# Kernel tuning notes

Measured on AMD Instinct MI355X. Metric: run time of the kernel, lower is better.

The kernel has to match this reference:

```python
import jax, jax.numpy as jnp
import numpy as np
import math

D_MODEL = 768
NHEAD = 12
NUM_LAYERS = 6
INPUT_DIM = 768
HEAD_DIM = D_MODEL // NHEAD
D_FF = 4 * D_MODEL
TOTAL_HEADS = NUM_LAYERS * NHEAD
B, N = 4, 512


def _ln(x, g, b, eps=1e-5):
    mu = jnp.mean(x, axis=-1, keepdims=True)
    var = jnp.mean((x - mu) ** 2, axis=-1, keepdims=True)
    return (x - mu) * jax.lax.rsqrt(var + eps) * g + b


def setup_inputs() -> dict:
    key = jax.random.key(0)
    ks = iter(jax.random.split(key, 32))
    s = 0.02  # init scale keeps sigmoid scores away from saturation
    d = {
        "sentence_embeddings": jax.random.normal(next(ks), (B, N, INPUT_DIM), jnp.float32),
        "Win": jax.random.normal(next(ks), (D_MODEL, INPUT_DIM), jnp.float32) * s,
        "b_in": jnp.zeros((D_MODEL,), jnp.float32),
        "Wq": jax.random.normal(next(ks), (NUM_LAYERS, D_MODEL, D_MODEL), jnp.float32) * s,
        "bq": jnp.zeros((NUM_LAYERS, D_MODEL), jnp.float32),
        "Wk": jax.random.normal(next(ks), (NUM_LAYERS, D_MODEL, D_MODEL), jnp.float32) * s,
        "bk": jnp.zeros((NUM_LAYERS, D_MODEL), jnp.float32),
        "Wv": jax.random.normal(next(ks), (NUM_LAYERS, D_MODEL, D_MODEL), jnp.float32) * s,
        "bv": jnp.zeros((NUM_LAYERS, D_MODEL), jnp.float32),
        "Wo": jax.random.normal(next(ks), (NUM_LAYERS, D_MODEL, D_MODEL), jnp.float32) * s,
        "bo": jnp.zeros((NUM_LAYERS, D_MODEL), jnp.float32),
        "g1": jnp.ones((NUM_LAYERS, D_MODEL), jnp.float32),
        "be1": jnp.zeros((NUM_LAYERS, D_MODEL), jnp.float32),
        "g2": jnp.ones((NUM_LAYERS, D_MODEL), jnp.float32),
        "be2": jnp.zeros((NUM_LAYERS, D_MODEL), jnp.float32),
        "W1": jax.random.normal(next(ks), (NUM_LAYERS, D_FF, D_MODEL), jnp.float32) * s,
        "bf1": jnp.zeros((NUM_LAYERS, D_FF), jnp.float32),
        "W2": jax.random.normal(next(ks), (NUM_LAYERS, D_MODEL, D_FF), jnp.float32) * s,
        "bf2": jnp.zeros((NUM_LAYERS, D_MODEL), jnp.float32),
        "Wr1": jax.random.normal(next(ks), (D_MODEL // 2, D_MODEL), jnp.float32) * s,
        "br1": jnp.zeros((D_MODEL // 2,), jnp.float32),
        "Wr2": jax.random.normal(next(ks), (TOTAL_HEADS, D_MODEL // 2), jnp.float32) * s,
        "br2": jnp.zeros((TOTAL_HEADS,), jnp.float32),
        "agg_bias": jnp.zeros((1,), jnp.float32),
    }
    return d


def _forward(sentence_embeddings, Win, b_in, Wq, bq, Wk, bk, Wv, bv, Wo, bo,
             g1, be1, g2, be2, W1, bf1, W2, bf2, Wr1, br1, Wr2, br2, agg_bias):
    b, n, _ = sentence_embeddings.shape
    x = sentence_embeddings @ Win.T + b_in  # [B,N,D]
    off_diag = (1.0 - jnp.eye(n, dtype=x.dtype))[None, None]  # [1,1,N,N]
    scale = 1.0 / math.sqrt(HEAD_DIM)
    all_scores = []
    for i in range(NUM_LAYERS):
        n1 = _ln(x, g1[i], be1[i])
        q = (n1 @ Wq[i].T + bq[i]).reshape(b, n, NHEAD, HEAD_DIM).transpose(0, 2, 1, 3)
        k = (n1 @ Wk[i].T + bk[i]).reshape(b, n, NHEAD, HEAD_DIM).transpose(0, 2, 1, 3)
        v = (n1 @ Wv[i].T + bv[i]).reshape(b, n, NHEAD, HEAD_DIM).transpose(0, 2, 1, 3)
        scores = jnp.einsum('bhnd,bhmd->bhnm', q, k) * scale
        probs = jax.nn.sigmoid(scores)  # [B,H,N,N]
        row_sums = probs.sum(axis=-1, keepdims=True) + 1e-6
        attn = jnp.einsum('bhnm,bhmd->bhnd', probs, v) / row_sums
        attn = attn.transpose(0, 2, 1, 3).reshape(b, n, D_MODEL)
        x = x + attn @ Wo[i].T + bo[i]
        n2 = _ln(x, g2[i], be2[i])
        ff = jax.nn.gelu(n2 @ W1[i].T + bf1[i], approximate=False) @ W2[i].T + bf2[i]
        x = x + ff
        all_scores.append(probs * off_diag)  # zero the diagonal
    raw_w = jax.nn.gelu(x @ Wr1.T + br1, approximate=False) @ Wr2.T + br2  # [B,N,LH]
    stacked = jnp.concatenate(all_scores, axis=1)  # [B, L*H, N, N]
    final = jnp.einsum('bnh,bhnm->bnm', raw_w, stacked)
    return final + agg_bias[0]


def reference(sentence_embeddings, Win, b_in, Wq, bq, Wk, bk, Wv, bv, Wo, bo,
              g1, be1, g2, be2, W1, bf1, W2, bf2, Wr1, br1, Wr2, br2, agg_bias):
    return _forward(sentence_embeddings, Win, b_in, Wq, bq, Wk, bk, Wv, bv, Wo, bo,
                    g1, be1, g2, be2, W1, bf1, W2, bf2, Wr1, br1, Wr2, br2, agg_bias)
```

## Files before the change

### kernel.cpp

```cpp
#include <hip/hip_runtime.h>
#include <stdint.h>

#define LAYERS 6
#define BB 4
#define NSEQ 512
#define DM 768
#define NH 12
#define HD 64
#define DFF 3072
#define MTOK 2048
#define QKVN 2304
#define DR1 384
#define TH 72

typedef __attribute__((ext_vector_type(8))) short bf16x8;
typedef __attribute__((ext_vector_type(4))) float f32x4;

__device__ __forceinline__ unsigned short f2bf(float f) {
  union { float f; uint32_t u; } v; v.f = f;
  return (unsigned short)((v.u + 0x7fffu + ((v.u >> 16) & 1u)) >> 16);
}
__device__ __forceinline__ float bf2f(unsigned short h) {
  union { uint32_t u; float f; } v; v.u = ((uint32_t)h) << 16;
  return v.f;
}
__device__ __forceinline__ void gload16(const void* g, void* l) {
  __builtin_amdgcn_global_load_lds((const __attribute__((address_space(1))) void*)g,
                                   (__attribute__((address_space(3))) void*)l, 16, 0, 0);
}
#define MFMA(a, b, c) __builtin_amdgcn_mfma_f32_16x16x32_bf16(a, b, c, 0, 0, 0)

__device__ __forceinline__ float sigmoid8(float s) {
  float e, r;
  float t = s * -0.18033688011112443f;
  asm("v_exp_f32 %0, %1" : "=v"(e) : "v"(t));
  float d = 1.0f + e;
  asm("v_rcp_f32 %0, %1" : "=v"(r) : "v"(d));
  return r;
}

__device__ __forceinline__ float gelu_f(float x) {
  float t = 0.7978845608028654f * x * (1.0f + 0.044715f * x * x);
  float u = fminf(t * 2.8853900817779268f, 126.0f);
  float e, r;
  asm("v_exp_f32 %0, %1" : "=v"(e) : "v"(u));
  float d = e + 1.0f;
  asm("v_rcp_f32 %0, %1" : "=v"(r) : "v"(d));
  return x * e * r;
}

__global__ void cvt_f32_bf16(const float* __restrict__ s, unsigned short* __restrict__ d, int n4) {
  int i = blockIdx.x * blockDim.x + threadIdx.x;
  if (i >= n4) return;
  float4 v = reinterpret_cast<const float4*>(s)[i];
  ushort4 o;
  o.x = f2bf(v.x); o.y = f2bf(v.y); o.z = f2bf(v.z); o.w = f2bf(v.w);
  reinterpret_cast<ushort4*>(d)[i] = o;
}

__global__ void convert_layer(const float* __restrict__ wq, const float* __restrict__ wk,
                              const float* __restrict__ wv, const float* __restrict__ wo,
                              const float* __restrict__ w1, const float* __restrict__ w2,
                              const float* __restrict__ bq, const float* __restrict__ bk,
                              const float* __restrict__ bv,
                              unsigned short* __restrict__ qkvw, float* __restrict__ qkvb,
                              unsigned short* __restrict__ wow, unsigned short* __restrict__ w1w,
                              unsigned short* __restrict__ w2w) {
  const int A4 = (QKVN * DM) / 4;
  const int B4 = (DM * DM) / 4;
  const int C4 = (DFF * DM) / 4;
  int i = blockIdx.x * blockDim.x + threadIdx.x;
  if (i < QKVN / 4) {
    int j = i * 4;
    #pragma unroll
    for (int t = 0; t < 4; ++t) {
      int jj = j + t;
      int seg = jj / DM, c = jj % DM;
      const float* src = (seg == 0) ? bq : ((seg == 1) ? bk : bv);
      qkvb[jj] = src[c];
    }
  }
  const float* s4; unsigned short* dst;
  if (i < A4) {
    int j = i * 4; int row = j / DM; int c = j % DM;
    const float* w = (row < DM) ? wq : ((row < 2 * DM) ? wk : wv);
    s4 = w + (size_t)(row % DM) * DM + c; dst = qkvw + j;
  } else if (i < A4 + B4) {
    int j = (i - A4) * 4; s4 = wo + j; dst = wow + j;
  } else if (i < A4 + B4 + C4) {
    int j = (i - A4 - B4) * 4; s4 = w1 + j; dst = w1w + j;
  } else if (i < A4 + B4 + 2 * C4) {
    int j = (i - A4 - B4 - C4) * 4; s4 = w2 + j; dst = w2w + j;
  } else return;
  float4 v = *reinterpret_cast<const float4*>(s4);
  ushort4 o;
  o.x = f2bf(v.x); o.y = f2bf(v.y); o.z = f2bf(v.z); o.w = f2bf(v.w);
  *reinterpret_cast<ushort4*>(dst) = o;
}

__global__ __launch_bounds__(256) void ln_kernel(const float* __restrict__ x,
                                                 const float* __restrict__ g,
                                                 const float* __restrict__ b,
                                                 unsigned short* __restrict__ out) {
  int wave = threadIdx.x >> 6;
  int lane = threadIdx.x & 63;
  int row = blockIdx.x * 4 + wave;
  const float* xr = x + (size_t)row * DM;
  float v[12];
  #pragma unroll
  for (int c = 0; c < 3; ++c) {
    float4 t = *reinterpret_cast<const float4*>(xr + lane * 12 + c * 4);
    v[c * 4 + 0] = t.x; v[c * 4 + 1] = t.y; v[c * 4 + 2] = t.z; v[c * 4 + 3] = t.w;
  }
  float s = 0.f, s2 = 0.f;
  #pragma unroll
  for (int c = 0; c < 12; ++c) { s += v[c]; s2 += v[c] * v[c]; }
  #pragma unroll
  for (int m = 1; m < 64; m <<= 1) { s += __shfl_xor(s, m); s2 += __shfl_xor(s2, m); }
  float mu = s * (1.f / 768.f);
  float var = s2 * (1.f / 768.f) - mu * mu;
  float rstd = rsqrtf(var + 1e-5f);
  unsigned short o[12];
  #pragma unroll
  for (int c = 0; c < 12; ++c) {
    int col = lane * 12 + c;
    o[c] = f2bf((v[c] - mu) * rstd * g[col] + b[col]);
  }
  unsigned short* orow = out + (size_t)row * DM + lane * 12;
  #pragma unroll
  for (int c = 0; c < 3; ++c)
    reinterpret_cast<ushort4*>(orow)[c] = make_ushort4(o[c * 4], o[c * 4 + 1], o[c * 4 + 2], o[c * 4 + 3]);
}

template<int BM, int BN, int EPI>
__global__ __launch_bounds__(256) void gemm_bt(const unsigned short* __restrict__ A,
                                               const unsigned short* __restrict__ B,
                                               const float* __restrict__ bias,
                                               const float* __restrict__ resid,
                                               float* __restrict__ outf,
                                               unsigned short* __restrict__ outb,
                                               int M, int N, int K) {
  constexpr int MI = BM / 32;
  constexpr int NI = BN / 32;
  constexpr int ACH = BM / 32;
  constexpr int BCH = BN / 32;
  __shared__ unsigned short As[2][BM * 64];
  __shared__ unsigned short Bs[2][BN * 64];
  const int tid = threadIdx.x;
  const int w = tid >> 6, lane = tid & 63;
  const int wr = w >> 1, wc = w & 1;
  const int l15 = lane & 15, rq = lane >> 4;
  const int bM = blockIdx.y * BM, bN = blockIdx.x * BN;
  const f32x4 zero4 = {0.f, 0.f, 0.f, 0.f};
  f32x4 acc[MI][NI];
  #pragma unroll
  for (int mi = 0; mi < MI; ++mi)
    #pragma unroll
    for (int ni = 0; ni < NI; ++ni) acc[mi][ni] = zero4;
  const int srow = lane >> 3;
  const int scol = ((lane & 7) ^ (lane >> 3)) * 8;
  auto stage = [&](int bf, int k0) {
    #pragma unroll
    for (int cc = 0; cc < ACH; ++cc) {
      int c = w * ACH + cc;
      gload16(A + (size_t)(bM + 8 * c + srow) * K + k0 + scol, (void*)(&As[bf][c * 512]));
    }
    #pragma unroll
    for (int cc = 0; cc < BCH; ++cc) {
      int c = w * BCH + cc;
      gload16(B + (size_t)(bN + 8 * c + srow) * K + k0 + scol, (void*)(&Bs[bf][c * 512]));
    }
  };
  const int kper = K / gridDim.z;
  const int kbase = blockIdx.z * kper;
  const int nt = kper / 64;
  stage(0, kbase);
  __syncthreads();
  int buf = 0;
  for (int t = 0; t < nt; ++t) {
    if (t + 1 < nt) stage(buf ^ 1, kbase + (t + 1) * 64);
    #pragma unroll
    for (int kk = 0; kk < 2; ++kk) {
      bf16x8 af[MI], bfr[NI];
      #pragma unroll
      for (int mi = 0; mi < MI; ++mi) {
        int row = wr * (BM / 2) + mi * 16 + l15;
        af[mi] = *(const bf16x8*)(&As[buf][row * 64 + (((kk * 4 + rq) ^ (row & 7)) * 8)]);
      }
      #pragma unroll
      for (int ni = 0; ni < NI; ++ni) {
        int row = wc * (BN / 2) + ni * 16 + l15;
        bfr[ni] = *(const bf16x8*)(&Bs[buf][row * 64 + (((kk * 4 + rq) ^ (row & 7)) * 8)]);
      }
      #pragma unroll
      for (int mi = 0; mi < MI; ++mi)
        #pragma unroll
        for (int ni = 0; ni < NI; ++ni)
          acc[mi][ni] = MFMA(af[mi], bfr[ni], acc[mi][ni]);
    }
    __syncthreads();
    buf ^= 1;
  }
  #pragma unroll
  for (int mi = 0; mi < MI; ++mi)
    #pragma unroll
    for (int ni = 0; ni < NI; ++ni)
      #pragma unroll
      for (int r = 0; r < 4; ++r) {
        int row = bM + wr * (BM / 2) + mi * 16 + 4 * rq + r;
        int col = bN + wc * (BN / 2) + ni * 16 + l15;
        if constexpr (EPI == 4) {
          outf[(size_t)blockIdx.z * M * N + (size_t)row * N + col] = acc[mi][ni][r];
        } else {
          float val = acc[mi][ni][r] + bias[col];
          if constexpr (EPI == 0) {
            outb[(size_t)row * N + col] = f2bf(val);
          } else if constexpr (EPI == 1) {
            outb[(size_t)row * N + col] = f2bf(gelu_f(val));
          } else if constexpr (EPI == 2) {
            outf[(size_t)row * N + col] = resid[(size_t)row * N + col] + val;
          } else {
            outf[(size_t)row * N + col] = val;
          }
        }
      }
}

__global__ __launch_bounds__(256) void ff2_combine(const float* __restrict__ pk,
                                                   const float* __restrict__ bias,
                                                   float* __restrict__ x,
                                                   unsigned short* __restrict__ xb) {
  int i = blockIdx.x * 256 + threadIdx.x;
  int e = i * 4;
  int col = e % DM;
  float4 a = *reinterpret_cast<const float4*>(x + e);
  float4 p0 = *reinterpret_cast<const float4*>(pk + e);
  float4 p1 = *reinterpret_cast<const float4*>(pk + (size_t)MTOK * DM + e);
  float4 b4 = *reinterpret_cast<const float4*>(bias + col);
  a.x += p0.x + p1.x + b4.x;
  a.y += p0.y + p1.y + b4.y;
  a.z += p0.z + p1.z + b4.z;
  a.w += p0.w + p1.w + b4.w;
  *reinterpret_cast<float4*>(x + e) = a;
  if (xb) {
    ushort4 o;
    o.x = f2bf(a.x); o.y = f2bf(a.y); o.z = f2bf(a.z); o.w = f2bf(a.w);
    *reinterpret_cast<ushort4*>(xb + e) = o;
  }
}

__global__ __launch_bounds__(256) void attn_kernel(const unsigned short* __restrict__ qkv,
                                                   float* __restrict__ po,
                                                   float* __restrict__ prs) {
  __shared__ unsigned short Ks[64 * 64];
  __shared__ unsigned short vt[64 * 72];
  __shared__ unsigned short pl[4][16 * 72];
  const int tid = threadIdx.x;
  const int w = tid >> 6, lane = tid & 63;
  const int l15 = lane & 15, rq = lane >> 4;
  const int b = blockIdx.y / NH, h = blockIdx.y % NH;
  const int n0 = blockIdx.x * 64;
  const int part = blockIdx.z;
  const unsigned short* base = qkv + (size_t)(b * NSEQ) * QKVN + h * HD;
  bf16x8 aq0, aq1;
  {
    const unsigned short* qp = base + (size_t)(n0 + w * 16 + l15) * QKVN + rq * 8;
    aq0 = *(const bf16x8*)qp;
    aq1 = *(const bf16x8*)(qp + 32);
  }
  float rs[4] = {0.f, 0.f, 0.f, 0.f};
  const f32x4 zero4 = {0.f, 0.f, 0.f, 0.f};
  f32x4 acco[4];
  #pragma unroll
  for (int j = 0; j < 4; ++j) acco[j] = zero4;
  unsigned short* plw = &pl[w][0];

  for (int mt = 0; mt < 4; ++mt) {
    const int m0 = part * 256 + mt * 64;
    __syncthreads();
    #pragma unroll
    for (int it = 0; it < 2; ++it) {
      int idx = tid + it * 256;
      int r = idx >> 3, c = idx & 7;
      bf16x8 kv = *(const bf16x8*)(base + 768 + (size_t)(m0 + r) * QKVN + c * 8);
      *(bf16x8*)(Ks + r * 64 + (c ^ (r & 7)) * 8) = kv;
      int cd = idx & 63, g = (idx >> 6) & 7;
      const unsigned short* vp = base + 1536 + (size_t)(m0 + g * 8) * QKVN + cd;
      bf16x8 vv;
      #pragma unroll
      for (int j = 0; j < 8; ++j) vv[j] = (short)vp[(size_t)j * QKVN];
      *(bf16x8*)(vt + cd * 72 + g * 8) = vv;
    }
    __syncthreads();
    #pragma unroll
    for (int ni = 0; ni < 4; ++ni) {
      int kr = ni * 16 + l15;
      bf16x8 bk0 = *(const bf16x8*)(Ks + kr * 64 + ((rq) ^ (kr & 7)) * 8);
      bf16x8 bk1 = *(const bf16x8*)(Ks + kr * 64 + ((rq + 4) ^ (kr & 7)) * 8);
      f32x4 z = zero4;
      z = MFMA(aq0, bk0, z);
      z = MFMA(aq1, bk1, z);
      #pragma unroll
      for (int r = 0; r < 4; ++r) {
        float p = sigmoid8(z[r]);
        rs[r] += p;
        plw[(4 * rq + r) * 72 + ni * 16 + l15] = f2bf(p);
      }
    }
    #pragma unroll
    for (int kk = 0; kk < 2; ++kk) {
      bf16x8 ap = *(const bf16x8*)(plw + l15 * 72 + kk * 32 + rq * 8);
      #pragma unroll
      for (int j2 = 0; j2 < 4; ++j2) {
        bf16x8 bvv = *(const bf16x8*)(vt + (j2 * 16 + l15) * 72 + kk * 32 + rq * 8);
        acco[j2] = MFMA(ap, bvv, acco[j2]);
      }
    }
  }
  #pragma unroll
  for (int m = 1; m < 16; m <<= 1)
    #pragma unroll
    for (int r = 0; r < 4; ++r) rs[r] += __shfl_xor(rs[r], m);
  float* pop = po + (size_t)part * MTOK * DM;
  #pragma unroll
  for (int j2 = 0; j2 < 4; ++j2)
    #pragma unroll
    for (int r = 0; r < 4; ++r) {
      int row = b * NSEQ + n0 + w * 16 + 4 * rq + r;
      int col = h * HD + j2 * 16 + l15;
      pop[(size_t)row * DM + col] = acco[j2][r];
    }
  if (l15 == 0) {
    #pragma unroll
    for (int r = 0; r < 4; ++r)
      prs[((size_t)part * (BB * NH) + blockIdx.y) * NSEQ + n0 + w * 16 + 4 * rq + r] = rs[r];
  }
}

__global__ __launch_bounds__(256) void attn_combine(const float* __restrict__ po,
                                                    const float* __restrict__ prs,
                                                    unsigned short* __restrict__ attnbf) {
  int i = blockIdx.x * 256 + threadIdx.x;
  int e = i * 4;
  int row = e / DM, col = e % DM;
  int b = row >> 9, n = row & 511, h = col >> 6;
  float r0 = prs[((size_t)(b * NH + h)) * NSEQ + n];
  float r1 = prs[(size_t)(BB * NH) * NSEQ + ((size_t)(b * NH + h)) * NSEQ + n];
  float inv = 1.f / (r0 + r1 + 1e-6f);
  float4 p0 = *reinterpret_cast<const float4*>(po + e);
  float4 p1 = *reinterpret_cast<const float4*>(po + (size_t)MTOK * DM + e);
  ushort4 o;
  o.x = f2bf((p0.x + p1.x) * inv);
  o.y = f2bf((p0.y + p1.y) * inv);
  o.z = f2bf((p0.z + p1.z) * inv);
  o.w = f2bf((p0.w + p1.w) * inv);
  *reinterpret_cast<ushort4*>(attnbf + e) = o;
}

__global__ __launch_bounds__(128) void wr2_kernel(const unsigned short* __restrict__ h1,
                                                  const float* __restrict__ wr2,
                                                  const float* __restrict__ br2,
                                                  float* __restrict__ raww) {
  __shared__ float hrow[DR1];
  int row = blockIdx.x;
  const unsigned short* hp = h1 + (size_t)row * DR1;
  for (int c = threadIdx.x; c < DR1; c += 128) hrow[c] = bf2f(hp[c]);
  __syncthreads();
  int j = threadIdx.x;
  if (j < TH) {
    const float* wrow = wr2 + (size_t)j * DR1;
    float acc = 0.f;
    for (int c = 0; c < DR1; ++c) acc += hrow[c] * wrow[c];
    raww[(size_t)row * TH + j] = acc + br2[j];
  }
}

__global__ __launch_bounds__(256) void agg_kernel(const unsigned short* __restrict__ qkv_all,
                                                  const float* __restrict__ raww,
                                                  float* __restrict__ part) {
  __shared__ unsigned short Ks[64 * 64];
  __shared__ unsigned short Qs[64 * 64];
  const int tid = threadIdx.x;
  const int w = tid >> 6, lane = tid & 63;
  const int l15 = lane & 15, rq = lane >> 4;
  const int z = blockIdx.z;
  const int l = z >> 2, b = z & 3;
  const int m0 = blockIdx.x * 64, nb = blockIdx.y * 64;
  const unsigned short* base = qkv_all + (size_t)l * MTOK * QKVN + (size_t)(b * NSEQ) * QKVN;
  const f32x4 zero4 = {0.f, 0.f, 0.f, 0.f};
  float acc[4][4];
  #pragma unroll
  for (int ni = 0; ni < 4; ++ni)
    #pragma unroll
    for (int r = 0; r < 4; ++r) acc[ni][r] = 0.f;
  for (int h = 0; h < NH; ++h) {
    __syncthreads();
    #pragma unroll
    for (int it = 0; it < 2; ++it) {
      int idx = tid + it * 256;
      int r = idx >> 3, c = idx & 7;
      bf16x8 kv = *(const bf16x8*)(base + (size_t)(m0 + r) * QKVN + 768 + h * HD + c * 8);
      *(bf16x8*)(Ks + r * 64 + (c ^ (r & 7)) * 8) = kv;
      bf16x8 qv = *(const bf16x8*)(base + (size_t)(nb + r) * QKVN + h * HD + c * 8);
      *(bf16x8*)(Qs + r * 64 + (c ^ (r & 7)) * 8) = qv;
    }
    __syncthreads();
    const int qr = w * 16 + l15;
    bf16x8 aq0 = *(const bf16x8*)(Qs + qr * 64 + ((rq) ^ (qr & 7)) * 8);
    bf16x8 aq1 = *(const bf16x8*)(Qs + qr * 64 + ((rq + 4) ^ (qr & 7)) * 8);
    float wl[4];
    #pragma unroll
    for (int r = 0; r < 4; ++r)
      wl[r] = raww[(size_t)(b * NSEQ + nb + w * 16 + 4 * rq + r) * TH + l * NH + h];
    #pragma unroll
    for (int ni = 0; ni < 4; ++ni) {
      int kr = ni * 16 + l15;
      bf16x8 bk0 = *(const bf16x8*)(Ks + kr * 64 + ((rq) ^ (kr & 7)) * 8);
      bf16x8 bk1 = *(const bf16x8*)(Ks + kr * 64 + ((rq + 4) ^ (kr & 7)) * 8);
      f32x4 zz = zero4;
      zz = MFMA(aq0, bk0, zz);
      zz = MFMA(aq1, bk1, zz);
      #pragma unroll
      for (int r = 0; r < 4; ++r) {
        acc[ni][r] += wl[r] * sigmoid8(zz[r]);
      }
    }
  }
  #pragma unroll
  for (int ni = 0; ni < 4; ++ni)
    #pragma unroll
    for (int r = 0; r < 4; ++r) {
      int n = nb + w * 16 + 4 * rq + r;
      part[((size_t)z * NSEQ + n) * NSEQ + m0 + ni * 16 + l15] = acc[ni][r];
    }
}

__global__ __launch_bounds__(256) void agg_reduce(const float* __restrict__ part,
                                                  const float* __restrict__ agg_bias,
                                                  float* __restrict__ out) {
  int i = blockIdx.x * 256 + threadIdx.x;
  int e = i * 4;
  float4 s = {0.f, 0.f, 0.f, 0.f};
  #pragma unroll
  for (int l = 0; l < LAYERS; ++l) {
    float4 p = *reinterpret_cast<const float4*>(part + (size_t)l * BB * NSEQ * NSEQ + e);
    s.x += p.x; s.y += p.y; s.z += p.z; s.w += p.w;
  }
  int n = (e >> 9) & 511, m = e & 511;
  float ab = agg_bias[0];
  float4 o;
  o.x = (n == m)     ? ab : s.x + ab;
  o.y = (n == m + 1) ? ab : s.y + ab;
  o.z = (n == m + 2) ? ab : s.z + ab;
  o.w = (n == m + 3) ? ab : s.w + ab;
  *reinterpret_cast<float4*>(out + e) = o;
}

extern "C" void kernel_launch(void* const* d_in, const int* in_sizes, int n_in,
                              void* d_out, int out_size, void* d_ws, size_t ws_size,
                              hipStream_t stream) {
  const float* emb  = (const float*)d_in[0];
  const float* Win  = (const float*)d_in[1];
  const float* b_in = (const float*)d_in[2];
  const float* Wq   = (const float*)d_in[3];
  const float* bq   = (const float*)d_in[4];
  const float* Wk   = (const float*)d_in[5];
  const float* bk   = (const float*)d_in[6];
  const float* Wv   = (const float*)d_in[7];
  const float* bv   = (const float*)d_in[8];
  const float* Wo   = (const float*)d_in[9];
  const float* bo   = (const float*)d_in[10];
  const float* g1   = (const float*)d_in[11];
  const float* be1  = (const float*)d_in[12];
  const float* g2   = (const float*)d_in[13];
  const float* be2  = (const float*)d_in[14];
  const float* W1   = (const float*)d_in[15];
  const float* bf1  = (const float*)d_in[16];
  const float* W2   = (const float*)d_in[17];
  const float* bf2  = (const float*)d_in[18];
  const float* Wr1  = (const float*)d_in[19];
  const float* br1  = (const float*)d_in[20];
  const float* Wr2  = (const float*)d_in[21];
  const float* br2  = (const float*)d_in[22];
  const float* aggb = (const float*)d_in[23];
  float* out = (float*)d_out;
  (void)in_sizes; (void)n_in; (void)out_size; (void)ws_size;

  char* ws = (char*)d_ws;
  size_t off = 0;
  auto alloc = [&](size_t bytes) -> char* {
    char* p = ws + off;
    off += (bytes + 255) & ~(size_t)255;
    return p;
  };
  unsigned short* qkvw   = (unsigned short*)alloc((size_t)QKVN * DM * 2);
  float*          qkvb   = (float*)alloc((size_t)QKVN * 4);
  unsigned short* wow    = (unsigned short*)alloc((size_t)DM * DM * 2);
  unsigned short* w1w    = (unsigned short*)alloc((size_t)DFF * DM * 2);
  unsigned short* w2w    = (unsigned short*)alloc((size_t)DM * DFF * 2);
  unsigned short* winw   = (unsigned short*)alloc((size_t)DM * DM * 2);
  unsigned short* wr1w   = (unsigned short*)alloc((size_t)DR1 * DM * 2);
  unsigned short* h1bf   = (unsigned short*)alloc((size_t)MTOK * DR1 * 2);
  float*          raww   = (float*)alloc((size_t)MTOK * TH * 4);
  float*          prs    = (float*)alloc((size_t)2 * BB * NH * NSEQ * 4);
  float*          skbuf  = (float*)alloc((size_t)2 * MTOK * DM * 4);
  unsigned short* qkvall = (unsigned short*)alloc((size_t)LAYERS * MTOK * QKVN * 2);
  char* scratch = alloc(0);
  unsigned short* embbf  = (unsigned short*)(scratch);
  float*          x      = (float*)(scratch + 3145728);
  unsigned short* nbf    = (unsigned short*)(scratch + 3145728 + 6291456);
  unsigned short* attnbf = (unsigned short*)(scratch + 3145728 + 6291456 + 3145728);
  char*           S      = scratch + 3145728 + 6291456 + 3145728 + 3145728;
  unsigned short* xbf    = (unsigned short*)(S + 12582912);
  float*          po     = (float*)S;
  unsigned short* ff1bf  = (unsigned short*)S;
  float*          part   = (float*)scratch;

  cvt_f32_bf16<<<1536, 256, 0, stream>>>(emb, embbf, (MTOK * DM) / 4);
  cvt_f32_bf16<<<576, 256, 0, stream>>>(Win, winw, (DM * DM) / 4);
  cvt_f32_bf16<<<288, 256, 0, stream>>>(Wr1, wr1w, (DR1 * DM) / 4);

  dim3 g768(DM / 64, MTOK / 64);
  gemm_bt<64, 64, 3><<<g768, 256, 0, stream>>>(embbf, winw, b_in, nullptr, x, nullptr, MTOK, DM, DM);

  const int CL_GRID = ((QKVN * DM + DM * DM + 2 * DFF * DM) / 4 + 255) / 256;
  for (int l = 0; l < LAYERS; ++l) {
    convert_layer<<<CL_GRID, 256, 0, stream>>>(
        Wq + (size_t)l * DM * DM, Wk + (size_t)l * DM * DM, Wv + (size_t)l * DM * DM,
        Wo + (size_t)l * DM * DM, W1 + (size_t)l * DFF * DM, W2 + (size_t)l * DM * DFF,
        bq + l * DM, bk + l * DM, bv + l * DM, qkvw, qkvb, wow, w1w, w2w);
    ln_kernel<<<512, 256, 0, stream>>>(x, g1 + l * DM, be1 + l * DM, nbf);
    unsigned short* qkvl = qkvall + (size_t)l * MTOK * QKVN;
    dim3 gqkv(QKVN / 128, MTOK / 128);
    gemm_bt<128, 128, 0><<<gqkv, 256, 0, stream>>>(nbf, qkvw, qkvb, nullptr, nullptr, qkvl, MTOK, QKVN, DM);
    attn_kernel<<<dim3(8, BB * NH, 2), 256, 0, stream>>>(qkvl, po, prs);
    attn_combine<<<(MTOK * DM / 4) / 256, 256, 0, stream>>>(po, prs, attnbf);
    gemm_bt<64, 64, 2><<<g768, 256, 0, stream>>>(attnbf, wow, bo + l * DM, x, x, nullptr, MTOK, DM, DM);
    ln_kernel<<<512, 256, 0, stream>>>(x, g2 + l * DM, be2 + l * DM, nbf);
    dim3 gff1(DFF / 128, MTOK / 128);
    gemm_bt<128, 128, 1><<<gff1, 256, 0, stream>>>(nbf, w1w, bf1 + l * DFF, nullptr, nullptr, ff1bf, MTOK, DFF, DM);
    dim3 gff2(DM / 64, MTOK / 64, 2);
    gemm_bt<64, 64, 4><<<gff2, 256, 0, stream>>>(ff1bf, w2w, nullptr, nullptr, skbuf, nullptr, MTOK, DM, DFF);
    ff2_combine<<<(MTOK * DM / 4) / 256, 256, 0, stream>>>(skbuf, bf2 + l * DM, x,
                                                          (l == LAYERS - 1) ? xbf : nullptr);
  }

  dim3 gr1(DR1 / 64, MTOK / 64);
  gemm_bt<64, 64, 1><<<gr1, 256, 0, stream>>>(xbf, wr1w, br1, nullptr, nullptr, h1bf, MTOK, DR1, DM);
  wr2_kernel<<<MTOK, 128, 0, stream>>>(h1bf, Wr2, br2, raww);
  agg_kernel<<<dim3(8, 8, LAYERS * BB), 256, 0, stream>>>(qkvall, raww, part);
  agg_reduce<<<(BB * NSEQ * NSEQ / 4) / 256, 256, 0, stream>>>(part, aggb, out);
}
```

Measured before the change: 755.5 us.

## Batch weight conversion, fuse FF2 combine with next LayerNorm, shrink GEMM tiles

Converts all six layers' weights to bf16 in one batched launch up front instead of one launch per layer, which needs per-layer weight buffers. Fuses the FF2 split-K combine and residual add with the next layer's LN1, dropping a kernel launch and an extra pass over x each layer. It also changes the QKV and FF1 GEMM tiles from 128x128 to 64x128 to get more blocks, and vectorizes the wr2 dot product with float4 loads. The risks are more workspace memory and lower per-block reuse from the smaller tiles.

```diff
diff --git a/kernel.cpp b/kernel.cpp
--- a/kernel.cpp
+++ b/kernel.cpp
@@ -58,17 +58,29 @@
   reinterpret_cast<ushort4*>(d)[i] = o;
 }
 
-__global__ void convert_layer(const float* __restrict__ wq, const float* __restrict__ wk,
-                              const float* __restrict__ wv, const float* __restrict__ wo,
-                              const float* __restrict__ w1, const float* __restrict__ w2,
-                              const float* __restrict__ bq, const float* __restrict__ bk,
-                              const float* __restrict__ bv,
-                              unsigned short* __restrict__ qkvw, float* __restrict__ qkvb,
-                              unsigned short* __restrict__ wow, unsigned short* __restrict__ w1w,
-                              unsigned short* __restrict__ w2w) {
+__global__ void convert_all(const float* __restrict__ Wq, const float* __restrict__ Wk,
+                            const float* __restrict__ Wv, const float* __restrict__ Wo,
+                            const float* __restrict__ W1, const float* __restrict__ W2,
+                            const float* __restrict__ bqA, const float* __restrict__ bkA,
+                            const float* __restrict__ bvA,
+                            unsigned short* __restrict__ qkvw6, float* __restrict__ qkvb6,
+                            unsigned short* __restrict__ wow6, unsigned short* __restrict__ w1w6,
+                            unsigned short* __restrict__ w2w6) {
   const int A4 = (QKVN * DM) / 4;
   const int B4 = (DM * DM) / 4;
   const int C4 = (DFF * DM) / 4;
+  const int l = blockIdx.y;
+  const float* wq = Wq + (size_t)l * DM * DM;
+  const float* wk = Wk + (size_t)l * DM * DM;
+  const float* wv = Wv + (size_t)l * DM * DM;
+  const float* wo = Wo + (size_t)l * DM * DM;
+  const float* w1 = W1 + (size_t)l * DFF * DM;
+  const float* w2 = W2 + (size_t)l * DM * DFF;
+  unsigned short* qkvw = qkvw6 + (size_t)l * QKVN * DM;
+  unsigned short* wow  = wow6  + (size_t)l * DM * DM;
+  unsigned short* w1w  = w1w6  + (size_t)l * DFF * DM;
+  unsigned short* w2w  = w2w6  + (size_t)l * DM * DFF;
+  float* qkvb = qkvb6 + (size_t)l * QKVN;
   int i = blockIdx.x * blockDim.x + threadIdx.x;
   if (i < QKVN / 4) {
     int j = i * 4;
@@ -76,7 +88,7 @@
     for (int t = 0; t < 4; ++t) {
       int jj = j + t;
       int seg = jj / DM, c = jj % DM;
-      const float* src = (seg == 0) ? bq : ((seg == 1) ? bk : bv);
+      const float* src = (seg == 0) ? (bqA + l * DM) : ((seg == 1) ? (bkA + l * DM) : (bvA + l * DM));
       qkvb[jj] = src[c];
     }
   }
@@ -127,6 +139,60 @@
     o[c] = f2bf((v[c] - mu) * rstd * g[col] + b[col]);
   }
   unsigned short* orow = out + (size_t)row * DM + lane * 12;
+  #pragma unroll
+  for (int c = 0; c < 3; ++c)
+    reinterpret_cast<ushort4*>(orow)[c] = make_ushort4(o[c * 4], o[c * 4 + 1], o[c * 4 + 2], o[c * 4 + 3]);
+}
+
+__global__ __launch_bounds__(256) void ff2_ln(const float* __restrict__ pk,
+                                              const float* __restrict__ bias,
+                                              float* __restrict__ x,
+                                              const float* __restrict__ g,
+                                              const float* __restrict__ b,
+                                              unsigned short* __restrict__ out,
+                                              int last) {
+  int wave = threadIdx.x >> 6;
+  int lane = threadIdx.x & 63;
+  int row = blockIdx.x * 4 + wave;
+  size_t base = (size_t)row * DM;
+  float v[12];
+  #pragma unroll
+  for (int c = 0; c < 3; ++c) {
+    int col = lane * 12 + c * 4;
+    float4 xv = *reinterpret_cast<const float4*>(x + base + col);
+    float4 p0 = *reinterpret_cast<const float4*>(pk + base + col);
+    float4 p1 = *reinterpret_cast<const float4*>(pk + (size_t)MTOK * DM + base + col);
+    float4 bb = *reinterpret_cast<const float4*>(bias + col);
+    v[c * 4 + 0] = xv.x + p0.x + p1.x + bb.x;
+    v[c * 4 + 1] = xv.y + p0.y + p1.y + bb.y;
+    v[c * 4 + 2] = xv.z + p0.z + p1.z + bb.z;
+    v[c * 4 + 3] = xv.w + p0.w + p1.w + bb.w;
+  }
+  #pragma unroll
+  for (int c = 0; c < 3; ++c) {
+    float4 o = {v[c * 4], v[c * 4 + 1], v[c * 4 + 2], v[c * 4 + 3]};
+    *reinterpret_cast<float4*>(x + base + lane * 12 + c * 4) = o;
+  }
+  unsigned short o[12];
+  if (last) {
+    #pragma unroll
+    for (int c = 0; c < 12; ++c) o[c] = f2bf(v[c]);
+  } else {
+    float s = 0.f, s2 = 0.f;
+    #pragma unroll
+    for (int c = 0; c < 12; ++c) { s += v[c]; s2 += v[c] * v[c]; }
+    #pragma unroll
+    for (int m = 1; m < 64; m <<= 1) { s += __shfl_xor(s, m); s2 += __shfl_xor(s2, m); }
+    float mu = s * (1.f / 768.f);
+    float var = s2 * (1.f / 768.f) - mu * mu;
+    float rstd = rsqrtf(var + 1e-5f);
+    #pragma unroll
+    for (int c = 0; c < 12; ++c) {
+      int col = lane * 12 + c;
+      o[c] = f2bf((v[c] - mu) * rstd * g[col] + b[col]);
+    }
+  }
+  unsigned short* orow = out + base + lane * 12;
   #pragma unroll
   for (int c = 0; c < 3; ++c)
     reinterpret_cast<ushort4*>(orow)[c] = make_ushort4(o[c * 4], o[c * 4 + 1], o[c * 4 + 2], o[c * 4 + 3]);
@@ -226,29 +292,6 @@
       }
 }
 
-__global__ __launch_bounds__(256) void ff2_combine(const float* __restrict__ pk,
-                                                   const float* __restrict__ bias,
-                                                   float* __restrict__ x,
-                                                   unsigned short* __restrict__ xb) {
-  int i = blockIdx.x * 256 + threadIdx.x;
-  int e = i * 4;
-  int col = e % DM;
-  float4 a = *reinterpret_cast<const float4*>(x + e);
-  float4 p0 = *reinterpret_cast<const float4*>(pk + e);
-  float4 p1 = *reinterpret_cast<const float4*>(pk + (size_t)MTOK * DM + e);
-  float4 b4 = *reinterpret_cast<const float4*>(bias + col);
-  a.x += p0.x + p1.x + b4.x;
-  a.y += p0.y + p1.y + b4.y;
-  a.z += p0.z + p1.z + b4.z;
-  a.w += p0.w + p1.w + b4.w;
-  *reinterpret_cast<float4*>(x + e) = a;
-  if (xb) {
-    ushort4 o;
-    o.x = f2bf(a.x); o.y = f2bf(a.y); o.z = f2bf(a.z); o.w = f2bf(a.w);
-    *reinterpret_cast<ushort4*>(xb + e) = o;
-  }
-}
-
 __global__ __launch_bounds__(256) void attn_kernel(const unsigned short* __restrict__ qkv,
                                                    float* __restrict__ po,
                                                    float* __restrict__ prs) {
@@ -370,7 +413,11 @@
   if (j < TH) {
     const float* wrow = wr2 + (size_t)j * DR1;
     float acc = 0.f;
-    for (int c = 0; c < DR1; ++c) acc += hrow[c] * wrow[c];
+    for (int c4 = 0; c4 < DR1 / 4; ++c4) {
+      float4 hv = *reinterpret_cast<const float4*>(hrow + c4 * 4);
+      float4 wv = *reinterpret_cast<const float4*>(wrow + c4 * 4);
+      acc += hv.x * wv.x + hv.y * wv.y + hv.z * wv.z + hv.w * wv.w;
+    }
     raww[(size_t)row * TH + j] = acc + br2[j];
   }
 }
@@ -493,11 +540,11 @@
     off += (bytes + 255) & ~(size_t)255;
     return p;
   };
-  unsigned short* qkvw   = (unsigned short*)alloc((size_t)QKVN * DM * 2);
-  float*          qkvb   = (float*)alloc((size_t)QKVN * 4);
-  unsigned short* wow    = (unsigned short*)alloc((size_t)DM * DM * 2);
-  unsigned short* w1w    = (unsigned short*)alloc((size_t)DFF * DM * 2);
-  unsigned short* w2w    = (unsigned short*)alloc((size_t)DM * DFF * 2);
+  unsigned short* qkvw6  = (unsigned short*)alloc((size_t)LAYERS * QKVN * DM * 2);
+  float*          qkvb6  = (float*)alloc((size_t)LAYERS * QKVN * 4);
+  unsigned short* wow6   = (unsigned short*)alloc((size_t)LAYERS * DM * DM * 2);
+  unsigned short* w1w6   = (unsigned short*)alloc((size_t)LAYERS * DFF * DM * 2);
+  unsigned short* w2w6   = (unsigned short*)alloc((size_t)LAYERS * DM * DFF * 2);
   unsigned short* winw   = (unsigned short*)alloc((size_t)DM * DM * 2);
   unsigned short* wr1w   = (unsigned short*)alloc((size_t)DR1 * DM * 2);
   unsigned short* h1bf   = (unsigned short*)alloc((size_t)MTOK * DR1 * 2);
@@ -520,29 +567,38 @@
   cvt_f32_bf16<<<576, 256, 0, stream>>>(Win, winw, (DM * DM) / 4);
   cvt_f32_bf16<<<288, 256, 0, stream>>>(Wr1, wr1w, (DR1 * DM) / 4);
 
+  const int CL_GRID = ((QKVN * DM + DM * DM + 2 * DFF * DM) / 4 + 255) / 256;
+  convert_all<<<dim3(CL_GRID, LAYERS), 256, 0, stream>>>(Wq, Wk, Wv, Wo, W1, W2, bq, bk, bv,
+                                                         qkvw6, qkvb6, wow6, w1w6, w2w6);
+
   dim3 g768(DM / 64, MTOK / 64);
   gemm_bt<64, 64, 3><<<g768, 256, 0, stream>>>(embbf, winw, b_in, nullptr, x, nullptr, MTOK, DM, DM);
-
-  const int CL_GRID = ((QKVN * DM + DM * DM + 2 * DFF * DM) / 4 + 255) / 256;
+  ln_kernel<<<512, 256, 0, stream>>>(x, g1, be1, nbf);
+
   for (int l = 0; l < LAYERS; ++l) {
-    convert_layer<<<CL_GRID, 256, 0, stream>>>(
-        Wq + (size_t)l * DM * DM, Wk + (size_t)l * DM * DM, Wv + (size_t)l * DM * DM,
-        Wo + (size_t)l * DM * DM, W1 + (size_t)l * DFF * DM, W2 + (size_t)l * DM * DFF,
-        bq + l * DM, bk + l * DM, bv + l * DM, qkvw, qkvb, wow, w1w, w2w);
-    ln_kernel<<<512, 256, 0, stream>>>(x, g1 + l * DM, be1 + l * DM, nbf);
     unsigned short* qkvl = qkvall + (size_t)l * MTOK * QKVN;
-    dim3 gqkv(QKVN / 128, MTOK / 128);
-    gemm_bt<128, 128, 0><<<gqkv, 256, 0, stream>>>(nbf, qkvw, qkvb, nullptr, nullptr, qkvl, MTOK, QKVN, DM);
+    dim3 gqkv(QKVN / 128, MTOK / 64);
+    gemm_bt<64, 128, 0><<<gqkv, 256, 0, stream>>>(nbf, qkvw6 + (size_t)l * QKVN * DM,
+                                                  qkvb6 + (size_t)l * QKVN, nullptr, nullptr,
+                                                  qkvl, MTOK, QKVN, DM);
     attn_kernel<<<dim3(8, BB * NH, 2), 256, 0, stream>>>(qkvl, po, prs);
     attn_combine<<<(MTOK * DM / 4) / 256, 256, 0, stream>>>(po, prs, attnbf);
-    gemm_bt<64, 64, 2><<<g768, 256, 0, stream>>>(attnbf, wow, bo + l * DM, x, x, nullptr, MTOK, DM, DM);
+    gemm_bt<64, 64, 2><<<g768, 256, 0, stream>>>(attnbf, wow6 + (size_t)l * DM * DM,
+                                                 bo + l * DM, x, x, nullptr, MTOK, DM, DM);
     ln_kernel<<<512, 256, 0, stream>>>(x, g2 + l * DM, be2 + l * DM, nbf);
-    dim3 gff1(DFF / 128, MTOK / 128);
-    gemm_bt<128, 128, 1><<<gff1, 256, 0, stream>>>(nbf, w1w, bf1 + l * DFF, nullptr, nullptr, ff1bf, MTOK, DFF, DM);
+    dim3 gff1(DFF / 128, MTOK / 64);
+    gemm_bt<64, 128, 1><<<gff1, 256, 0, stream>>>(nbf, w1w6 + (size_t)l * DFF * DM,
+                                                  bf1 + l * DFF, nullptr, nullptr, ff1bf,
+                                                  MTOK, DFF, DM);
     dim3 gff2(DM / 64, MTOK / 64, 2);
-    gemm_bt<64, 64, 4><<<gff2, 256, 0, stream>>>(ff1bf, w2w, nullptr, nullptr, skbuf, nullptr, MTOK, DM, DFF);
-    ff2_combine<<<(MTOK * DM / 4) / 256, 256, 0, stream>>>(skbuf, bf2 + l * DM, x,
-                                                          (l == LAYERS - 1) ? xbf : nullptr);
+    gemm_bt<64, 64, 4><<<gff2, 256, 0, stream>>>(ff1bf, w2w6 + (size_t)l * DM * DFF,
+                                                 nullptr, nullptr, skbuf, nullptr, MTOK, DM, DFF);
+    if (l < LAYERS - 1) {
+      ff2_ln<<<512, 256, 0, stream>>>(skbuf, bf2 + l * DM, x,
+                                      g1 + (l + 1) * DM, be1 + (l + 1) * DM, nbf, 0);
+    } else {
+      ff2_ln<<<512, 256, 0, stream>>>(skbuf, bf2 + l * DM, x, g1, be1, xbf, 1);
+    }
   }
 
   dim3 gr1(DR1 / 64, MTOK / 64);
```

Result: faster. 707.4 us (-6.4%).
